# Kernel optimization log

Hardware: AMD Instinct MI355X
Metric: run time of the kernel (lower is better)

Reference implementation:

```python
import jax, jax.numpy as jnp
import numpy as np

NUM_GRAPHS = 64

def setup_inputs() -> dict:
    key = jax.random.key(0)
    ks = jax.random.split(key, 10)
    N, E, D, V = 100000, 1600000, 64, 30
    node_types = jax.random.randint(ks[0], (N,), 0, V, dtype=jnp.int64 if jax.config.jax_enable_x64 else jnp.int32)
    edge_index = jax.random.randint(ks[1], (2, E), 0, N, dtype=jnp.int32)
    batch = jnp.sort(jax.random.randint(ks[2], (N,), 0, NUM_GRAPHS, dtype=jnp.int32))
    emb_table = jax.random.normal(ks[3], (V, D), dtype=jnp.float32)
    W1 = jax.random.normal(ks[4], (D, D), dtype=jnp.float32) / np.sqrt(D)
    W2 = jax.random.normal(ks[5], (D, D), dtype=jnp.float32) / np.sqrt(D)
    W3 = jax.random.normal(ks[6], (D, D), dtype=jnp.float32) / np.sqrt(D)
    b1 = jnp.zeros((D,), jnp.float32)
    b2 = jnp.zeros((D,), jnp.float32)
    b3 = jnp.zeros((D,), jnp.float32)
    return {"node_types": node_types, "edge_index": edge_index, "batch": batch,
            "emb_table": emb_table, "W1": W1, "b1": b1, "W2": W2, "b2": b2, "W3": W3, "b3": b3}

def _gcn_conv(x, W, b, row, col, norm, N):
    # x' = D^-1/2 (A+I) D^-1/2 (x @ W) + b   (PyG GCNConv semantics)
    h = x @ W
    msg = h[row] * norm[:, None]              # gather + edgewise scale
    out = jax.ops.segment_sum(msg, col, num_segments=N)  # scatter-add at targets
    return out + b

def reference(node_types, edge_index, batch, emb_table, W1, b1, W2, b2, W3, b3):
    N = node_types.shape[0]
    # add self-loops
    loops = jnp.arange(N, dtype=edge_index.dtype)
    row = jnp.concatenate([edge_index[0], loops])
    col = jnp.concatenate([edge_index[1], loops])
    # symmetric normalization on A + I
    deg = jax.ops.segment_sum(jnp.ones_like(col, dtype=jnp.float32), col, num_segments=N)
    dinv = jnp.where(deg > 0, jax.lax.rsqrt(deg), 0.0)
    norm = dinv[row] * dinv[col]
    x = emb_table[node_types]
    x = jax.nn.relu(_gcn_conv(x, W1, b1, row, col, norm, N))
    x = jax.nn.relu(_gcn_conv(x, W2, b2, row, col, norm, N))
    x = _gcn_conv(x, W3, b3, row, col, norm, N)
    # global mean pool over batch segments
    sums = jax.ops.segment_sum(x, batch, num_segments=NUM_GRAPHS)
    cnts = jax.ops.segment_sum(jnp.ones((N,), jnp.float32), batch, num_segments=NUM_GRAPHS)
    pooled = sums / jnp.maximum(cnts, 1.0)[:, None]
    # L2 normalize rows
    return pooled / jnp.linalg.norm(pooled, axis=1, keepdims=True)
```

## Files before the change

### kernel.cpp

```cpp
#include <hip/hip_runtime.h>
#include <hip/hip_fp16.h>

#define DD 64
#define NUM_GRAPHS 64
#define AGG_BLOCKS 2048
#define EB 512
#define BINW 128
#define BINSH 7
#define MAXNB 1024
#define EBIN_CAP 3072
#define SPAD 64

typedef _Float16 h2_t __attribute__((ext_vector_type(2)));

__device__ __forceinline__ float fdot2u(unsigned a, unsigned b, float c) {
    return __builtin_amdgcn_fdot2(__builtin_bit_cast(h2_t, a),
                                  __builtin_bit_cast(h2_t, b), c, false);
}

#define MDLO(m) __half2float(__ushort_as_half((unsigned short)((m) & 0xFFFF)))

__device__ __forceinline__ float fmixlo(float a, unsigned r) {
    float o;
    asm("v_fma_mix_f32 %0, %1, 1.0, %2 op_sel_hi:[1,0,0]"
        : "=v"(o) : "v"(r), "v"(a));
    return o;
}
__device__ __forceinline__ float fmixhi(float a, unsigned r) {
    float o;
    asm("v_fma_mix_f32 %0, %1, 1.0, %2 op_sel:[1,0,0] op_sel_hi:[1,0,0]"
        : "=v"(o) : "v"(r), "v"(a));
    return o;
}

__global__ __launch_bounds__(256) void k_hist(const int* __restrict__ col,
                                              int* __restrict__ H, int E, int NB, int CE) {
    __shared__ int h[MAXNB];
    int eb = blockIdx.x, t = threadIdx.x;
    for (int i = t; i < NB; i += 256) h[i] = 0;
    __syncthreads();
    int e0 = eb * CE, e1 = min(E, e0 + CE);
    for (int e = e0 + t; e < e1; e += 256) atomicAdd(&h[col[e] >> BINSH], 1);
    __syncthreads();
    for (int i = t; i < NB; i += 256) H[eb * NB + i] = h[i];
}

__global__ __launch_bounds__(256) void k_scanA(int* __restrict__ H,
                                               int* __restrict__ bintot, int NB) {
    __shared__ int s[256];
    int b = blockIdx.x, t = threadIdx.x;
    int i0 = (2 * t) * NB + b, i1 = (2 * t + 1) * NB + b;
    int v0 = H[i0], v1 = H[i1];
    int tot = v0 + v1;
    s[t] = tot;
    __syncthreads();
    for (int off = 1; off < 256; off <<= 1) {
        int tv = (t >= off) ? s[t - off] : 0;
        __syncthreads();
        s[t] += tv;
        __syncthreads();
    }
    int excl = s[t] - tot;
    H[i0] = excl;
    H[i1] = excl + v0;
    if (t == 255) bintot[b] = s[255];
}

__global__ void k_scanB(const int* __restrict__ bintot, int* __restrict__ binstart, int NB) {
    __shared__ int s[512];
    int t = threadIdx.x;
    int i0 = 2 * t, i1 = 2 * t + 1;
    int v0 = (i0 < NB) ? bintot[i0] : 0;
    int v1 = (i1 < NB) ? bintot[i1] : 0;
    int tot = v0 + v1;
    s[t] = tot;
    __syncthreads();
    for (int off = 1; off < 512; off <<= 1) {
        int tv = (t >= off) ? s[t - off] : 0;
        __syncthreads();
        s[t] += tv;
        __syncthreads();
    }
    int excl = s[t] - tot;
    if (i0 < NB) binstart[i0] = excl;
    if (i1 < NB) binstart[i1] = excl + v0;
    if (t == 511) binstart[NB] = s[511];
}

__global__ __launch_bounds__(256) void k_scatbin(const int* __restrict__ row,
                                                 const int* __restrict__ col,
                                                 const int* __restrict__ H,
                                                 const int* __restrict__ binstart,
                                                 unsigned* __restrict__ binned,
                                                 int E, int NB, int CE) {
    __shared__ int off[MAXNB];
    int eb = blockIdx.x, t = threadIdx.x;
    for (int i = t; i < NB; i += 256) off[i] = binstart[i] + H[eb * NB + i];
    __syncthreads();
    int e0 = eb * CE, e1 = min(E, e0 + CE);
    for (int e = e0 + t; e < e1; e += 256) {
        int c = col[e], r = row[e];
        int slot = atomicAdd(&off[c >> BINSH], 1);
        binned[slot] = ((unsigned)(c & (BINW - 1)) << 24) | (unsigned)r;
    }
}

__global__ __launch_bounds__(256) void k_bincsr(const unsigned* __restrict__ binned,
                                                const int* __restrict__ binstart,
                                                const int* __restrict__ nt,
                                                int* __restrict__ srcidx,
                                                int* __restrict__ rowptr,
                                                float* __restrict__ dinv,
                                                int2* __restrict__ pk, int N, int NB) {
    __shared__ unsigned arr[EBIN_CAP];
    __shared__ int sorted_[EBIN_CAP];
    __shared__ int cnt[BINW];
    __shared__ int base[BINW];
    __shared__ int cursor[BINW];
    int b = blockIdx.x, t = threadIdx.x;
    int s0 = binstart[b], s1 = binstart[b + 1];
    int binsz = s1 - s0;
    if (binsz > EBIN_CAP) binsz = EBIN_CAP;
    if (t < BINW) cnt[t] = 0;
    __syncthreads();
    for (int i = t; i < binsz; i += 256) {
        unsigned val = binned[s0 + i];
        arr[i] = val;
        atomicAdd(&cnt[val >> 24], 1);
    }
    __syncthreads();
    int v = (t < BINW) ? cnt[t] : 0;
    float di = rsqrtf((float)v + 1.0f);
    if (t < BINW) base[t] = v;
    __syncthreads();
    for (int off = 1; off < BINW; off <<= 1) {
        int tv = (t >= off && t < BINW) ? base[t - off] : 0;
        __syncthreads();
        if (t < BINW) base[t] += tv;
        __syncthreads();
    }
    int excl = (t < BINW) ? (base[t] - v) : 0;
    __syncthreads();
    if (t < BINW) { base[t] = excl; cursor[t] = excl; }
    __syncthreads();
    for (int i = t; i < binsz; i += 256) {
        unsigned val = arr[i];
        int pos = atomicAdd(&cursor[val >> 24], 1);
        sorted_[pos] = (int)(val & 0xFFFFFF);
    }
    __syncthreads();
    for (int i = t; i < binsz; i += 256) srcidx[s0 + i] = sorted_[i];
    int node = b * BINW + t;
    if (t < BINW && node < N) {
        rowptr[node] = s0 + base[t];
        dinv[node] = di;
        pk[node] = make_int2(nt[node], __float_as_int(di));
    }
    if (b == NB - 1 && t == 0) rowptr[N] = s1;
}

__global__ void k_buildepk(const int* __restrict__ srcidx, const int2* __restrict__ pk,
                           unsigned* __restrict__ epku, int E) {
    int i = blockIdx.x * blockDim.x + threadIdx.x;
    if (i >= E) return;
    int2 p = pk[srcidx[i]];
    epku[i] = ((unsigned)p.x << 16) |
              (unsigned)__half_as_ushort(__float2half(__int_as_float(p.y)));
}

__global__ void k_embW1(const float* __restrict__ emb, const float* __restrict__ W1,
                        float* __restrict__ embW1, int V) {
    __shared__ float er[DD];
    int v = blockIdx.x, j = threadIdx.x;
    er[j] = emb[v * DD + j];
    __syncthreads();
    float acc = 0.0f;
    #pragma unroll
    for (int d = 0; d < DD; ++d) acc += er[d] * W1[d * DD + j];
    embW1[v * DD + j] = acc;
}

__global__ void k_packW(const float* __restrict__ W, unsigned* __restrict__ Wpk) {
    int t = blockIdx.x * blockDim.x + threadIdx.x;
    if (t >= 32 * DD) return;
    int p = t >> 6, j = t & 63;
    __half2 h = __floats2half2_rn(W[(2 * p) * DD + j], W[(2 * p + 1) * DD + j]);
    Wpk[t] = __builtin_bit_cast(unsigned, h);
}

__device__ __forceinline__ void acc_h4(float4& a, uint2 r) {
    a.x = fmixlo(a.x, r.x); a.y = fmixhi(a.y, r.x);
    a.z = fmixlo(a.z, r.y); a.w = fmixhi(a.w, r.y);
}

__device__ __forceinline__ float4 gather_partial_q(const int* __restrict__ srcidx,
                                                   const __half* __restrict__ Hs,
                                                   int s, int e, int g, int l) {
    float4 A = {0,0,0,0}, B = {0,0,0,0}, C = {0,0,0,0}, D = {0,0,0,0};
    int k = s;
    int kend = s + ((e - s) & ~15);
    if (k < kend) {
        uint2 r0 = *(const uint2*)(Hs + (long)srcidx[k + g] * DD + 4 * l);
        uint2 r1 = *(const uint2*)(Hs + (long)srcidx[k + 4 + g] * DD + 4 * l);
        uint2 r2 = *(const uint2*)(Hs + (long)srcidx[k + 8 + g] * DD + 4 * l);
        uint2 r3 = *(const uint2*)(Hs + (long)srcidx[k + 12 + g] * DD + 4 * l);
        k += 16;
        for (; k < kend; k += 16) {
            uint2 n0 = *(const uint2*)(Hs + (long)srcidx[k + g] * DD + 4 * l);
            uint2 n1 = *(const uint2*)(Hs + (long)srcidx[k + 4 + g] * DD + 4 * l);
            uint2 n2 = *(const uint2*)(Hs + (long)srcidx[k + 8 + g] * DD + 4 * l);
            uint2 n3 = *(const uint2*)(Hs + (long)srcidx[k + 12 + g] * DD + 4 * l);
            acc_h4(A, r0); acc_h4(B, r1); acc_h4(C, r2); acc_h4(D, r3);
            r0 = n0; r1 = n1; r2 = n2; r3 = n3;
        }
        acc_h4(A, r0); acc_h4(B, r1); acc_h4(C, r2); acc_h4(D, r3);
    }
    for (; k < e; k += 4) {
        if (k + g < e) {
            uint2 rr = *(const uint2*)(Hs + (long)srcidx[k + g] * DD + 4 * l);
            acc_h4(A, rr);
        }
    }
    A.x += B.x + C.x + D.x; A.y += B.y + C.y + D.y;
    A.z += B.z + C.z + D.z; A.w += B.w + C.w + D.w;
    return A;
}

__device__ __forceinline__ void acc_h8(float4& A, float4& B, uint4 r) {
    float2 f0 = __half22float2(*(const __half2*)&r.x);
    float2 f1 = __half22float2(*(const __half2*)&r.y);
    float2 f2 = __half22float2(*(const __half2*)&r.z);
    float2 f3 = __half22float2(*(const __half2*)&r.w);
    A.x += f0.x; A.y += f0.y; A.z += f1.x; A.w += f1.y;
    B.x += f2.x; B.y += f2.y; B.z += f3.x; B.w += f3.y;
}

__device__ __forceinline__ void gather_sum_8p(const int* __restrict__ srcidx,
                                              const __half* __restrict__ Hs,
                                              int s, int e, int g, int l,
                                              float4& A, float4& B,
                                              int pi0, int pi1, int pi2, int pi3) {
    float4 A1 = {0.f, 0.f, 0.f, 0.f}, B1 = {0.f, 0.f, 0.f, 0.f};
    int k = s;
    int kend = s + ((e - s) & ~15);
    if (k < kend) {
        uint4 r0 = *(const uint4*)(Hs + (long)pi0 * DD + 8 * l);
        uint4 r1 = *(const uint4*)(Hs + (long)pi1 * DD + 8 * l);
        k += 16;
        for (; k < kend; k += 16) {
            uint4 n0 = *(const uint4*)(Hs + (long)srcidx[k + g] * DD + 8 * l);
            uint4 n1 = *(const uint4*)(Hs + (long)srcidx[k + 8 + g] * DD + 8 * l);
            acc_h8(A, B, r0);
            acc_h8(A1, B1, r1);
            r0 = n0; r1 = n1;
        }
        acc_h8(A, B, r0);
        acc_h8(A1, B1, r1);
    }
    if (k + 8 <= e) {
        uint4 r = *(const uint4*)(Hs + (long)pi2 * DD + 8 * l);
        acc_h8(A, B, r);
        k += 8;
        pi2 = pi3;
    }
    if (k + g < e) {
        uint4 r = *(const uint4*)(Hs + (long)pi2 * DD + 8 * l);
        acc_h8(A1, B1, r);
    }
    A.x += A1.x; A.y += A1.y; A.z += A1.z; A.w += A1.w;
    B.x += B1.x; B.y += B1.y; B.z += B1.z; B.w += B1.w;
}

__global__ __launch_bounds__(256, 4) void k_agg1_fused(const int* __restrict__ rowptr,
                                                    const unsigned* __restrict__ epku,
                                                    const int2* __restrict__ pk,
                                                    const float* __restrict__ embW1,
                                                    const float* __restrict__ b1,
                                                    __half* __restrict__ OUT, int N, int V) {
    __shared__ float ew[30 * DD];
    int tid = threadIdx.x;
    for (int k = tid; k < V * DD; k += 256) ew[k] = embW1[k];
    __syncthreads();
    int lane = tid & 63;
    int g = lane >> 4, l = lane & 15;
    float4 bq = *(const float4*)(b1 + 4 * l);
    int wstride = gridDim.x * 4;
    int node = __builtin_amdgcn_readfirstlane(blockIdx.x * 4 + (tid >> 6));
    int s = 0, e = 0;
    unsigned pu0 = 0, pu1 = 0, pu2 = 0, pu3 = 0;
    if (node < N) {
        s = rowptr[node]; e = rowptr[node + 1];
        int q1 = s + ((e - s) & ~7);
        pu0 = epku[s + g];  pu1 = epku[s + 4 + g];
        pu2 = epku[q1 + g]; pu3 = epku[q1 + 4 + g];
    }
#define P8(U0, U1) { \
        unsigned _u0 = (U0), _u1 = (U1); \
        int _t0 = _u0 >> 16, _t1 = _u1 >> 16; \
        float _d0 = MDLO(_u0), _d1 = MDLO(_u1); \
        float4 _w0 = *(const float4*)(ew + _t0 * DD + 4 * l); \
        float4 _w1 = *(const float4*)(ew + _t1 * DD + 4 * l); \
        acc.x += _w0.x * _d0 + _w1.x * _d1; \
        acc.y += _w0.y * _d0 + _w1.y * _d1; \
        acc.z += _w0.z * _d0 + _w1.z * _d1; \
        acc.w += _w0.w * _d0 + _w1.w * _d1; }
#define P4(U0) { \
        unsigned _u0 = (U0); \
        int _t0 = _u0 >> 16; \
        float _d0 = MDLO(_u0); \
        float4 _w0 = *(const float4*)(ew + _t0 * DD + 4 * l); \
        acc.x += _w0.x * _d0; acc.y += _w0.y * _d0; \
        acc.z += _w0.z * _d0; acc.w += _w0.w * _d0; }
    while (node < N) {
        int nn = node + wstride;
        int ns = 0, ne = 0;
        if (nn < N) { ns = rowptr[nn]; ne = rowptr[nn + 1]; }
        int2 pc = pk[node];
        float4 acc = {0.f, 0.f, 0.f, 0.f};
        int k = s;
        if (k + 8 <= e) {
            P8(pu0, pu1);
            k += 8;
            for (; k + 8 <= e; k += 8) P8(epku[k + g], epku[k + 4 + g]);
        }
        if (k + 4 <= e) { P4(pu2); k += 4; pu2 = pu3; }
        if (k + g < e)  { P4(pu2); }
        unsigned npu0 = 0, npu1 = 0, npu2 = 0, npu3 = 0;
        if (nn < N) {
            int q1 = ns + ((ne - ns) & ~7);
            npu0 = epku[ns + g];  npu1 = epku[ns + 4 + g];
            npu2 = epku[q1 + g];  npu3 = epku[q1 + 4 + g];
        }
        acc.x += __shfl_xor(acc.x, 16, 64); acc.x += __shfl_xor(acc.x, 32, 64);
        acc.y += __shfl_xor(acc.y, 16, 64); acc.y += __shfl_xor(acc.y, 32, 64);
        acc.z += __shfl_xor(acc.z, 16, 64); acc.z += __shfl_xor(acc.z, 32, 64);
        acc.w += __shfl_xor(acc.w, 16, 64); acc.w += __shfl_xor(acc.w, 32, 64);
        float dc = __int_as_float(pc.y);
        float4 wc = *(const float4*)(ew + pc.x * DD + 4 * l);
        float4 v;
        v.x = fmaxf((acc.x + wc.x * dc) * dc + bq.x, 0.f) * dc;
        v.y = fmaxf((acc.y + wc.y * dc) * dc + bq.y, 0.f) * dc;
        v.z = fmaxf((acc.z + wc.z * dc) * dc + bq.z, 0.f) * dc;
        v.w = fmaxf((acc.w + wc.w * dc) * dc + bq.w, 0.f) * dc;
        if (g == 0) {
            __half2 h0 = __floats2half2_rn(v.x, v.y);
            __half2 h1 = __floats2half2_rn(v.z, v.w);
            uint2 st;
            st.x = __builtin_bit_cast(unsigned, h0);
            st.y = __builtin_bit_cast(unsigned, h1);
            *(uint2*)(OUT + (long)node * DD + 4 * l) = st;
        }
        node = nn; s = ns; e = ne;
        pu0 = npu0; pu1 = npu1; pu2 = npu2; pu3 = npu3;
    }
#undef P8
#undef P4
}

__global__ __launch_bounds__(256, 4) void k_agg2_fused(const int* __restrict__ rowptr,
                                                    const int* __restrict__ srcidx,
                                                    const float* __restrict__ dinv,
                                                    const __half* __restrict__ Hs,
                                                    const float* __restrict__ b2,
                                                    const unsigned* __restrict__ W2pk,
                                                    __half* __restrict__ OUT, int N) {
    int tid = threadIdx.x;
    int lane = tid & 63;
    int g = lane >> 3, l = lane & 7;
    unsigned Wc[32];
    #pragma unroll
    for (int p = 0; p < 32; ++p) Wc[p] = W2pk[p * DD + lane];
    float bl = b2[lane];
    int wstride = gridDim.x * 4;
    int node = __builtin_amdgcn_readfirstlane(blockIdx.x * 4 + (tid >> 6));
    int s = 0, e = 0;
    int pi0 = 0, pi1 = 0, pi2 = 0, pi3 = 0;
    if (node < N) {
        s = rowptr[node]; e = rowptr[node + 1];
        int q = s + ((e - s) & ~15);
        pi0 = srcidx[s + g];  pi1 = srcidx[s + 8 + g];
        pi2 = srcidx[q + g];  pi3 = srcidx[q + 8 + g];
    }
    while (node < N) {
        int nn = node + wstride;
        int ns = 0, ne = 0;
        if (nn < N) { ns = rowptr[nn]; ne = rowptr[nn + 1]; }
        float dc = dinv[node];
        uint4 sr = *(const uint4*)(Hs + (long)node * DD + 8 * l);
        float4 A = {0.f, 0.f, 0.f, 0.f}, B = {0.f, 0.f, 0.f, 0.f};
        gather_sum_8p(srcidx, Hs, s, e, g, l, A, B, pi0, pi1, pi2, pi3);
        int npi0 = 0, npi1 = 0, npi2 = 0, npi3 = 0;
        if (nn < N) {
            int qn = ns + ((ne - ns) & ~15);
            npi0 = srcidx[ns + g];  npi1 = srcidx[ns + 8 + g];
            npi2 = srcidx[qn + g];  npi3 = srcidx[qn + 8 + g];
        }
        #pragma unroll
        for (int m = 8; m <= 32; m <<= 1) {
            A.x += __shfl_xor(A.x, m, 64); A.y += __shfl_xor(A.y, m, 64);
            A.z += __shfl_xor(A.z, m, 64); A.w += __shfl_xor(A.w, m, 64);
            B.x += __shfl_xor(B.x, m, 64); B.y += __shfl_xor(B.y, m, 64);
            B.z += __shfl_xor(B.z, m, 64); B.w += __shfl_xor(B.w, m, 64);
        }
        float2 s0 = __half22float2(*(const __half2*)&sr.x);
        float2 s1 = __half22float2(*(const __half2*)&sr.y);
        float2 s2 = __half22float2(*(const __half2*)&sr.z);
        float2 s3 = __half22float2(*(const __half2*)&sr.w);
        float t0 = (A.x + s0.x) * dc, t1 = (A.y + s0.y) * dc;
        float t2 = (A.z + s1.x) * dc, t3 = (A.w + s1.y) * dc;
        float t4 = (B.x + s2.x) * dc, t5 = (B.y + s2.y) * dc;
        float t6 = (B.z + s3.x) * dc, t7 = (B.w + s3.y) * dc;
        int vp0 = __builtin_bit_cast(int, __floats2half2_rn(t0, t1));
        int vp1 = __builtin_bit_cast(int, __floats2half2_rn(t2, t3));
        int vp2 = __builtin_bit_cast(int, __floats2half2_rn(t4, t5));
        int vp3 = __builtin_bit_cast(int, __floats2half2_rn(t6, t7));
        float o0 = 0.f, o1 = 0.f, o2 = 0.f, o3 = 0.f;
        #pragma unroll
        for (int p = 0; p < 32; p += 4) {
            o0 = fdot2u((unsigned)__builtin_amdgcn_readlane(vp0, p >> 2), Wc[p + 0], o0);
            o1 = fdot2u((unsigned)__builtin_amdgcn_readlane(vp1, p >> 2), Wc[p + 1], o1);
            o2 = fdot2u((unsigned)__builtin_amdgcn_readlane(vp2, p >> 2), Wc[p + 2], o2);
            o3 = fdot2u((unsigned)__builtin_amdgcn_readlane(vp3, p >> 2), Wc[p + 3], o3);
        }
        float u = (o0 + o1) + (o2 + o3);
        float v2 = fmaxf(u + bl, 0.f);
        OUT[(long)node * DD + lane] = __float2half(v2 * dc);
        node = nn; s = ns; e = ne;
        pi0 = npi0; pi1 = npi1; pi2 = npi2; pi3 = npi3;
    }
}

__device__ __forceinline__ void flush_pool_q(float4& PA, float* __restrict__ pool,
                                             int gcur, int g, int l) {
    gcur &= (NUM_GRAPHS - 1);
    PA.x += __shfl_xor(PA.x, 16, 64); PA.x += __shfl_xor(PA.x, 32, 64);
    PA.y += __shfl_xor(PA.y, 16, 64); PA.y += __shfl_xor(PA.y, 32, 64);
    PA.z += __shfl_xor(PA.z, 16, 64); PA.z += __shfl_xor(PA.z, 32, 64);
    PA.w += __shfl_xor(PA.w, 16, 64); PA.w += __shfl_xor(PA.w, 32, 64);
    if (g == 0) {
        atomicAdd(&pool[gcur * DD + 4 * l + 0], PA.x);
        atomicAdd(&pool[gcur * DD + 4 * l + 1], PA.y);
        atomicAdd(&pool[gcur * DD + 4 * l + 2], PA.z);
        atomicAdd(&pool[gcur * DD + 4 * l + 3], PA.w);
    }
}

__global__ __launch_bounds__(256, 4) void k_agg3_pool(const int* __restrict__ rowptr,
                                                   const int* __restrict__ srcidx,
                                                   const float* __restrict__ dinv,
                                                   const __half* __restrict__ Hs,
                                                   const int* __restrict__ batch,
                                                   float* __restrict__ pool,
                                                   int N, int chunk) {
    int tid = threadIdx.x;
    int lane = tid & 63;
    int g = lane >> 4, l = lane & 15;
    int w = __builtin_amdgcn_readfirstlane(blockIdx.x * 4 + (tid >> 6));
    int start = w * chunk;
    if (start >= N) return;
    int endn = min(N, start + chunk);
    int gcur = batch[start];
    float4 PA = {0.f, 0.f, 0.f, 0.f};
    int s = rowptr[start];
    for (int node = start; node < endn; ++node) {
        int e = rowptr[node + 1];
        float dc = dinv[node];
        int gb = batch[node];
        uint2 sr = *(const uint2*)(Hs + (long)node * DD + 4 * l);
        float4 A = gather_partial_q(srcidx, Hs, s, e, g, l);
        if (g == 0) {
            A.x = fmixlo(A.x, sr.x); A.y = fmixhi(A.y, sr.x);
            A.z = fmixlo(A.z, sr.y); A.w = fmixhi(A.w, sr.y);
        }
        if (gb != gcur) {
            flush_pool_q(PA, pool, gcur, g, l);
            gcur = gb;
            PA.x = dc * A.x; PA.y = dc * A.y; PA.z = dc * A.z; PA.w = dc * A.w;
        } else {
            PA.x += dc * A.x; PA.y += dc * A.y; PA.z += dc * A.z; PA.w += dc * A.w;
        }
        s = e;
    }
    flush_pool_q(PA, pool, gcur, g, l);
}

__global__ void k_final(const float* __restrict__ pool, const int* __restrict__ batch,
                        const float* __restrict__ W3, const float* __restrict__ b3,
                        float* __restrict__ out, int N) {
    __shared__ float pr[DD];
    int g = blockIdx.x, j = threadIdx.x;
    pr[j] = pool[g * DD + j];
    __syncthreads();
    int lo = 0, hi = N;
    while (lo < hi) { int m = (lo + hi) >> 1; if (batch[m] < g) lo = m + 1; else hi = m; }
    int lo2 = lo; hi = N;
    while (lo2 < hi) { int m = (lo2 + hi) >> 1; if (batch[m] < g + 1) lo2 = m + 1; else hi = m; }
    float cnt = fmaxf((float)(lo2 - lo), 1.0f);
    float acc = 0.0f;
    #pragma unroll
    for (int d = 0; d < DD; ++d) acc += pr[d] * W3[d * DD + j];
    float v = acc / cnt + b3[j];
    float sq = v * v;
    #pragma unroll
    for (int off = 32; off > 0; off >>= 1) sq += __shfl_down(sq, off, 64);
    float nrm = __shfl(sq, 0, 64);
    out[g * DD + j] = v / sqrtf(nrm);
}

extern "C" void kernel_launch(void* const* d_in, const int* in_sizes, int n_in,
                              void* d_out, int out_size, void* d_ws, size_t ws_size,
                              hipStream_t stream) {
    const int*   node_types = (const int*)d_in[0];
    const int*   edge_index = (const int*)d_in[1];
    const int*   batch      = (const int*)d_in[2];
    const float* emb        = (const float*)d_in[3];
    const float* W1 = (const float*)d_in[4];
    const float* b1 = (const float*)d_in[5];
    const float* W2 = (const float*)d_in[6];
    const float* b2 = (const float*)d_in[7];
    const float* W3 = (const float*)d_in[8];
    const float* b3 = (const float*)d_in[9];
    const int N = in_sizes[0];
    const int E = in_sizes[1] / 2;
    const int V = in_sizes[3] / DD;
    const int* row = edge_index;
    const int* col = edge_index + E;
    const long ND = (long)N * DD;
    const int NB = (N + BINW - 1) / BINW;
    const int CE = (E + EB - 1) / EB;

    char* p = (char*)d_ws;
    __half*   hsA     = (__half*)p;       p += ND * sizeof(__half);
    __half*   hsB     = (__half*)p;       p += ND * sizeof(__half);
    int*      srcidx  = (int*)p;          p += (size_t)(E + SPAD) * sizeof(int);
    unsigned* epku    = (unsigned*)p;     p += (size_t)(E + SPAD) * sizeof(unsigned);
    unsigned* binned  = (unsigned*)p;     p += (size_t)E * sizeof(unsigned);
    int*      H       = (int*)p;          p += (size_t)EB * NB * sizeof(int);
    int*      bintot  = (int*)p;          p += (size_t)(NB + 4) * sizeof(int);
    int*      binstart= (int*)p;          p += (size_t)(NB + 4) * sizeof(int);
    float*    dinv    = (float*)p;        p += (size_t)N * sizeof(float);
    int2*     pk      = (int2*)p;         p += (size_t)N * sizeof(int2);
    int*      rowptr  = (int*)p;          p += (size_t)(N + 4) * sizeof(int);
    float*    pool    = (float*)p;        p += (size_t)NUM_GRAPHS * DD * sizeof(float);
    float*    embW1   = (float*)p;        p += (size_t)V * DD * sizeof(float);
    unsigned* W2pk    = (unsigned*)p;     p += 32 * DD * sizeof(unsigned);

    hipMemsetAsync(srcidx + E, 0, SPAD * sizeof(int), stream);

    k_hist<<<EB, 256, 0, stream>>>(col, H, E, NB, CE);
    k_scanA<<<NB, 256, 0, stream>>>(H, bintot, NB);
    k_scanB<<<1, 512, 0, stream>>>(bintot, binstart, NB);
    k_scatbin<<<EB, 256, 0, stream>>>(row, col, H, binstart, binned, E, NB, CE);
    k_bincsr<<<NB, 256, 0, stream>>>(binned, binstart, node_types, srcidx, rowptr,
                                     dinv, pk, N, NB);
    k_buildepk<<<(E + 255) / 256, 256, 0, stream>>>(srcidx, pk, epku, E);

    k_embW1<<<V, DD, 0, stream>>>(emb, W1, embW1, V);
    k_packW<<<8, 256, 0, stream>>>(W2, W2pk);

    k_agg1_fused<<<AGG_BLOCKS, 256, 0, stream>>>(rowptr, epku, pk, embW1, b1,
                                                 hsA, N, V);
    k_agg2_fused<<<AGG_BLOCKS, 256, 0, stream>>>(rowptr, srcidx, dinv, hsA, b2, W2pk,
                                                 hsB, N);
    hipMemsetAsync(pool, 0, (size_t)(NUM_GRAPHS * DD) * sizeof(float), stream);
    const int totalWaves = AGG_BLOCKS * 4;
    const int chunk = (N + totalWaves - 1) / totalWaves;
    k_agg3_pool<<<AGG_BLOCKS, 256, 0, stream>>>(rowptr, srcidx, dinv, hsB, batch,
                                                pool, N, chunk);
    k_final<<<NUM_GRAPHS, DD, 0, stream>>>(pool, batch, W3, b3, (float*)d_out, N);
}
```

Measured before the change: 268.3 us.

## Prefetch next node's first gather rows in agg2 and fold memsets into kernels

In the layer-2 aggregation kernel, the first two feature rows for the next node are now loaded during the current node's epilogue rather than only their indices, so more gather latency overlaps with the shuffle reduction and matvec. The two hipMemsetAsync calls (srcidx padding and pool zeroing) are moved into existing kernels (scanB and buildepk), which removes two stream operations and their launch overhead. The deeper prefetch raises register pressure in a kernel with launch bounds of 4 blocks per CU and could cause spills.

```diff
diff --git a/kernel.cpp b/kernel.cpp
--- a/kernel.cpp
+++ b/kernel.cpp
@@ -66,9 +66,11 @@
     if (t == 255) bintot[b] = s[255];
 }
 
-__global__ void k_scanB(const int* __restrict__ bintot, int* __restrict__ binstart, int NB) {
+__global__ void k_scanB(const int* __restrict__ bintot, int* __restrict__ binstart,
+                        int* __restrict__ srcidx, int E, int NB) {
     __shared__ int s[512];
     int t = threadIdx.x;
+    if (t < SPAD) srcidx[E + t] = 0;
     int i0 = 2 * t, i1 = 2 * t + 1;
     int v0 = (i0 < NB) ? bintot[i0] : 0;
     int v1 = (i1 < NB) ? bintot[i1] : 0;
@@ -160,8 +162,9 @@
 }
 
 __global__ void k_buildepk(const int* __restrict__ srcidx, const int2* __restrict__ pk,
-                           unsigned* __restrict__ epku, int E) {
+                           unsigned* __restrict__ epku, float* __restrict__ pool, int E) {
     int i = blockIdx.x * blockDim.x + threadIdx.x;
+    if (i < NUM_GRAPHS * DD) pool[i] = 0.f;
     if (i >= E) return;
     int2 p = pk[srcidx[i]];
     epku[i] = ((unsigned)p.x << 16) |
@@ -235,17 +238,15 @@
     B.x += f2.x; B.y += f2.y; B.z += f3.x; B.w += f3.y;
 }
 
-__device__ __forceinline__ void gather_sum_8p(const int* __restrict__ srcidx,
+__device__ __forceinline__ void gather_sum_8r(const int* __restrict__ srcidx,
                                               const __half* __restrict__ Hs,
                                               int s, int e, int g, int l,
                                               float4& A, float4& B,
-                                              int pi0, int pi1, int pi2, int pi3) {
+                                              uint4 r0, uint4 r1, int pi2, int pi3) {
     float4 A1 = {0.f, 0.f, 0.f, 0.f}, B1 = {0.f, 0.f, 0.f, 0.f};
     int k = s;
     int kend = s + ((e - s) & ~15);
     if (k < kend) {
-        uint4 r0 = *(const uint4*)(Hs + (long)pi0 * DD + 8 * l);
-        uint4 r1 = *(const uint4*)(Hs + (long)pi1 * DD + 8 * l);
         k += 16;
         for (; k < kend; k += 16) {
             uint4 n0 = *(const uint4*)(Hs + (long)srcidx[k + g] * DD + 8 * l);
@@ -374,12 +375,15 @@
     int wstride = gridDim.x * 4;
     int node = __builtin_amdgcn_readfirstlane(blockIdx.x * 4 + (tid >> 6));
     int s = 0, e = 0;
-    int pi0 = 0, pi1 = 0, pi2 = 0, pi3 = 0;
+    int pi2 = 0, pi3 = 0;
+    uint4 cr0 = {0, 0, 0, 0}, cr1 = {0, 0, 0, 0};
     if (node < N) {
         s = rowptr[node]; e = rowptr[node + 1];
         int q = s + ((e - s) & ~15);
-        pi0 = srcidx[s + g];  pi1 = srcidx[s + 8 + g];
+        int i0 = srcidx[s + g], i1 = srcidx[s + 8 + g];
         pi2 = srcidx[q + g];  pi3 = srcidx[q + 8 + g];
+        cr0 = *(const uint4*)(Hs + (long)i0 * DD + 8 * l);
+        cr1 = *(const uint4*)(Hs + (long)i1 * DD + 8 * l);
     }
     while (node < N) {
         int nn = node + wstride;
@@ -388,12 +392,15 @@
         float dc = dinv[node];
         uint4 sr = *(const uint4*)(Hs + (long)node * DD + 8 * l);
         float4 A = {0.f, 0.f, 0.f, 0.f}, B = {0.f, 0.f, 0.f, 0.f};
-        gather_sum_8p(srcidx, Hs, s, e, g, l, A, B, pi0, pi1, pi2, pi3);
-        int npi0 = 0, npi1 = 0, npi2 = 0, npi3 = 0;
+        gather_sum_8r(srcidx, Hs, s, e, g, l, A, B, cr0, cr1, pi2, pi3);
+        int npi2 = 0, npi3 = 0;
+        uint4 nr0 = {0, 0, 0, 0}, nr1 = {0, 0, 0, 0};
         if (nn < N) {
             int qn = ns + ((ne - ns) & ~15);
-            npi0 = srcidx[ns + g];  npi1 = srcidx[ns + 8 + g];
+            int i0 = srcidx[ns + g], i1 = srcidx[ns + 8 + g];
             npi2 = srcidx[qn + g];  npi3 = srcidx[qn + 8 + g];
+            nr0 = *(const uint4*)(Hs + (long)i0 * DD + 8 * l);
+            nr1 = *(const uint4*)(Hs + (long)i1 * DD + 8 * l);
         }
         #pragma unroll
         for (int m = 8; m <= 32; m <<= 1) {
@@ -426,7 +433,7 @@
         float v2 = fmaxf(u + bl, 0.f);
         OUT[(long)node * DD + lane] = __float2half(v2 * dc);
         node = nn; s = ns; e = ne;
-        pi0 = npi0; pi1 = npi1; pi2 = npi2; pi3 = npi3;
+        pi2 = npi2; pi3 = npi3; cr0 = nr0; cr1 = nr1;
     }
 }
 
@@ -545,15 +552,13 @@
     float*    embW1   = (float*)p;        p += (size_t)V * DD * sizeof(float);
     unsigned* W2pk    = (unsigned*)p;     p += 32 * DD * sizeof(unsigned);
 
-    hipMemsetAsync(srcidx + E, 0, SPAD * sizeof(int), stream);
-
     k_hist<<<EB, 256, 0, stream>>>(col, H, E, NB, CE);
     k_scanA<<<NB, 256, 0, stream>>>(H, bintot, NB);
-    k_scanB<<<1, 512, 0, stream>>>(bintot, binstart, NB);
+    k_scanB<<<1, 512, 0, stream>>>(bintot, binstart, srcidx, E, NB);
     k_scatbin<<<EB, 256, 0, stream>>>(row, col, H, binstart, binned, E, NB, CE);
     k_bincsr<<<NB, 256, 0, stream>>>(binned, binstart, node_types, srcidx, rowptr,
                                      dinv, pk, N, NB);
-    k_buildepk<<<(E + 255) / 256, 256, 0, stream>>>(srcidx, pk, epku, E);
+    k_buildepk<<<(E + 255) / 256, 256, 0, stream>>>(srcidx, pk, epku, pool, E);
 
     k_embW1<<<V, DD, 0, stream>>>(emb, W1, embW1, V);
     k_packW<<<8, 256, 0, stream>>>(W2, W2pk);
@@ -562,7 +567,6 @@
                                                  hsA, N, V);
     k_agg2_fused<<<AGG_BLOCKS, 256, 0, stream>>>(rowptr, srcidx, dinv, hsA, b2, W2pk,
                                                  hsB, N);
-    hipMemsetAsync(pool, 0, (size_t)(NUM_GRAPHS * DD) * sizeof(float), stream);
     const int totalWaves = AGG_BLOCKS * 4;
     const int chunk = (N + totalWaves - 1) / totalWaves;
     k_agg3_pool<<<AGG_BLOCKS, 256, 0, stream>>>(rowptr, srcidx, dinv, hsB, batch,
```

Measured after the change: 270.8 us. No clear change (+0.9%).
